# Kernel optimization log

Measured on AMD Instinct MI355X. Metric: run time of the kernel, lower is better.

The kernel has to match this reference:

```python
import jax, jax.numpy as jnp
import numpy as np

N = 50000      # nodes
E = 200000     # edges (before self-loops)
D_IN = 256
HID = 128
NEG_SLOPE = 0.2
BN_EPS = 1e-5


def _lin(k, fan_in, fan_out):
    return jax.random.normal(k, (fan_in, fan_out), jnp.float32) / np.float32(np.sqrt(fan_in))


def setup_inputs() -> dict:
    key = jax.random.key(0)
    ks = jax.random.split(key, 40)
    d = {}
    d['x'] = jax.random.normal(ks[0], (N, D_IN), jnp.float32)
    d['edge_index'] = jax.random.randint(ks[1], (2, E), 0, N, dtype=jnp.int32)
    # GAT layer 1: 256 -> 128, heads=4 (concat -> 512)
    d['W1'] = _lin(ks[2], D_IN, 4 * HID)
    d['asrc1'] = jax.random.normal(ks[3], (4, HID), jnp.float32) * 0.1
    d['adst1'] = jax.random.normal(ks[4], (4, HID), jnp.float32) * 0.1
    d['b1'] = jnp.zeros((4 * HID,), jnp.float32)
    d['g1'] = jax.random.uniform(ks[5], (4 * HID,), jnp.float32, 0.5, 1.5)
    d['be1'] = jax.random.normal(ks[6], (4 * HID,), jnp.float32) * 0.1
    d['m1'] = jax.random.normal(ks[7], (4 * HID,), jnp.float32) * 0.1
    d['v1'] = jax.random.uniform(ks[8], (4 * HID,), jnp.float32, 0.5, 1.5)
    # GAT layer 2: 512 -> 128, heads=4 (concat -> 512)
    d['W2'] = _lin(ks[9], 4 * HID, 4 * HID)
    d['asrc2'] = jax.random.normal(ks[10], (4, HID), jnp.float32) * 0.1
    d['adst2'] = jax.random.normal(ks[11], (4, HID), jnp.float32) * 0.1
    d['b2'] = jnp.zeros((4 * HID,), jnp.float32)
    d['g2'] = jax.random.uniform(ks[12], (4 * HID,), jnp.float32, 0.5, 1.5)
    d['be2'] = jax.random.normal(ks[13], (4 * HID,), jnp.float32) * 0.1
    d['m2'] = jax.random.normal(ks[14], (4 * HID,), jnp.float32) * 0.1
    d['v2'] = jax.random.uniform(ks[15], (4 * HID,), jnp.float32, 0.5, 1.5)
    # GAT layer 3: 512 -> 128, heads=1
    d['W3'] = _lin(ks[16], 4 * HID, HID)
    d['asrc3'] = jax.random.normal(ks[17], (1, HID), jnp.float32) * 0.1
    d['adst3'] = jax.random.normal(ks[18], (1, HID), jnp.float32) * 0.1
    d['b3'] = jnp.zeros((HID,), jnp.float32)
    d['g3'] = jax.random.uniform(ks[19], (HID,), jnp.float32, 0.5, 1.5)
    d['be3'] = jax.random.normal(ks[20], (HID,), jnp.float32) * 0.1
    d['m3'] = jax.random.normal(ks[21], (HID,), jnp.float32) * 0.1
    d['v3'] = jax.random.uniform(ks[22], (HID,), jnp.float32, 0.5, 1.5)
    # classifier head: 128 -> 64 -> 10
    d['Wc1'] = _lin(ks[23], HID, HID // 2)
    d['bc1'] = jnp.zeros((HID // 2,), jnp.float32)
    d['Wc2'] = _lin(ks[24], HID // 2, 10)
    d['bc2'] = jnp.zeros((10,), jnp.float32)
    return d


def _gat_layer(h, src, dst, W, asrc, adst, b, heads, ch):
    # PyG GATConv (eval mode): linear -> per-head scores -> segment softmax over dst -> aggregate
    xp = (h @ W).reshape(-1, heads, ch)                 # [N, H, C]
    e_src = (xp * asrc[None]).sum(-1)                   # [N, H]
    e_dst = (xp * adst[None]).sum(-1)                   # [N, H]
    e = jax.nn.leaky_relu(e_src[src] + e_dst[dst], NEG_SLOPE)  # [E', H]
    m = jax.lax.stop_gradient(jax.ops.segment_max(e, dst, num_segments=N))
    w = jnp.exp(e - m[dst])
    s = jax.ops.segment_sum(w, dst, num_segments=N)     # [N, H]
    alpha = w / (s[dst] + 1e-16)                        # [E', H]
    out = jax.ops.segment_sum(alpha[:, :, None] * xp[src], dst, num_segments=N)  # [N, H, C]
    return out.reshape(-1, heads * ch) + b


def _bn_relu(h, g, be, mu, var):
    return jax.nn.relu((h - mu) * jax.lax.rsqrt(var + BN_EPS) * g + be)


def reference(x, edge_index,
              W1, asrc1, adst1, b1, g1, be1, m1, v1,
              W2, asrc2, adst2, b2, g2, be2, m2, v2,
              W3, asrc3, adst3, b3, g3, be3, m3, v3,
              Wc1, bc1, Wc2, bc2):
    loop = jnp.arange(N, dtype=edge_index.dtype)
    src = jnp.concatenate([edge_index[0], loop])        # GATConv adds self-loops
    dst = jnp.concatenate([edge_index[1], loop])
    h = _bn_relu(_gat_layer(x, src, dst, W1, asrc1, adst1, b1, 4, HID), g1, be1, m1, v1)
    h = _bn_relu(_gat_layer(h, src, dst, W2, asrc2, adst2, b2, 4, HID), g2, be2, m2, v2)
    h = _bn_relu(_gat_layer(h, src, dst, W3, asrc3, adst3, b3, 1, HID), g3, be3, m3, v3)
    E_GNN = h                                           # [N, 128]
    logits = jax.nn.relu(E_GNN @ Wc1 + bc1) @ Wc2 + bc2 # [N, 10]
    P_GNN = jax.nn.softmax(logits, axis=-1)
    return (E_GNN, P_GNN)
```

## Files before the change

kernel.cpp:

```cpp
#include <hip/hip_runtime.h>
#include <math.h>

#define N_NODES 50000
#define N_EDGES 200000
#define NEG_SLOPE 0.2f
#define BN_EPS 1e-5f

#define SCAN_ELEMS 1024
#define SCAN_NB ((N_NODES + SCAN_ELEMS - 1) / SCAN_ELEMS)

typedef __attribute__((ext_vector_type(4))) float f32x4;
typedef __attribute__((ext_vector_type(8))) short bf16x8;
typedef __attribute__((ext_vector_type(8))) ushort u16x8;
typedef __attribute__((ext_vector_type(2))) ushort u16x2;

__device__ __forceinline__ ushort f2bf(float x) {
    unsigned u = __float_as_uint(x);
    u += 0x7FFFu + ((u >> 16) & 1u);
    return (ushort)(u >> 16);
}
__device__ __forceinline__ float bf2f(ushort u) {
    return __uint_as_float(((unsigned)u) << 16);
}

__global__ void k_init(int* cnt, int* off) {
    int i = blockIdx.x * blockDim.x + threadIdx.x;
    if (i < N_NODES) { cnt[i] = 1; off[i] = 1; }
}

__global__ void k_count(const int* __restrict__ ei, int* cnt) {
    int e = blockIdx.x * blockDim.x + threadIdx.x;
    if (e < N_EDGES) atomicAdd(&cnt[ei[N_EDGES + e]], 1);
}

__global__ __launch_bounds__(256) void k_scan1(const int* __restrict__ cnt,
                                               int* __restrict__ incl,
                                               int* __restrict__ partials) {
    __shared__ int sh[256];
    const int t = threadIdx.x;
    const int base = blockIdx.x * SCAN_ELEMS + t * 4;
    int v0 = 0, v1 = 0, v2 = 0, v3 = 0;
    if (base + 3 < N_NODES) {
        int4 lv = *reinterpret_cast<const int4*>(&cnt[base]);
        v0 = lv.x; v1 = lv.y; v2 = lv.z; v3 = lv.w;
    } else {
        if (base + 0 < N_NODES) v0 = cnt[base + 0];
        if (base + 1 < N_NODES) v1 = cnt[base + 1];
        if (base + 2 < N_NODES) v2 = cnt[base + 2];
        if (base + 3 < N_NODES) v3 = cnt[base + 3];
    }
    const int s1 = v0 + v1, s2 = s1 + v2, s3 = s2 + v3;
    sh[t] = s3;
    __syncthreads();
#pragma unroll
    for (int off = 1; off < 256; off <<= 1) {
        int x = (t >= off) ? sh[t - off] : 0;
        __syncthreads();
        sh[t] += x;
        __syncthreads();
    }
    const int excl = sh[t] - s3;
    if (base + 0 < N_NODES) incl[base + 0] = excl + v0;
    if (base + 1 < N_NODES) incl[base + 1] = excl + s1;
    if (base + 2 < N_NODES) incl[base + 2] = excl + s2;
    if (base + 3 < N_NODES) incl[base + 3] = excl + s3;
    if (t == 255) partials[blockIdx.x] = sh[255];
}

__global__ void k_scan2(const int* __restrict__ partials, int* __restrict__ pofs) {
    if (threadIdx.x == 0) {
        int s = 0;
        for (int b = 0; b < SCAN_NB; ++b) { pofs[b] = s; s += partials[b]; }
    }
}

__global__ void k_scan3(const int* __restrict__ incl, const int* __restrict__ pofs,
                        int* __restrict__ row_ptr) {
    int i = blockIdx.x * blockDim.x + threadIdx.x;
    if (i < N_NODES) row_ptr[i + 1] = incl[i] + pofs[i >> 10];
    if (i == 0) row_ptr[0] = 0;
}

__global__ void k_self(const int* __restrict__ row_ptr, int* colb) {
    int n = blockIdx.x * blockDim.x + threadIdx.x;
    if (n < N_NODES) colb[row_ptr[n]] = n;
}

__global__ void k_scatter(const int* __restrict__ ei, const int* __restrict__ row_ptr,
                          int* off, int* colb) {
    int e = blockIdx.x * blockDim.x + threadIdx.x;
    if (e < N_EDGES) {
        int dst = ei[N_EDGES + e];
        int p = atomicAdd(&off[dst], 1);
        colb[row_ptr[dst] + p] = ei[e];
    }
}

__global__ void k_cvt(const float* __restrict__ in, ushort* __restrict__ out, int n4) {
    int i = blockIdx.x * blockDim.x + threadIdx.x;
    if (i < n4) {
        float4 v = reinterpret_cast<const float4*>(in)[i];
        ushort4 o;
        o.x = f2bf(v.x); o.y = f2bf(v.y); o.z = f2bf(v.z); o.w = f2bf(v.w);
        reinterpret_cast<ushort4*>(out)[i] = o;
    }
}

__global__ void k_wt(const float* __restrict__ W, ushort* __restrict__ Wt, int K, int N) {
    int idx = blockIdx.x * blockDim.x + threadIdx.x;
    if (idx < K * N) {
        int n = idx / K, k = idx - n * K;
        Wt[idx] = f2bf(W[(size_t)k * N + n]);
    }
}

__global__ __launch_bounds__(512) void k_gemm256(const ushort* __restrict__ A,
                                                 const ushort* __restrict__ Bt,
                                                 ushort* __restrict__ Cb,
                                                 const float* __restrict__ asrc,
                                                 const float* __restrict__ adst,
                                                 float* __restrict__ es,
                                                 float* __restrict__ ed,
                                                 int M, int K) {
    constexpr int N = 512;
    __shared__ __align__(16) ushort L[2][12288];
    __shared__ float sles[4][128];
    __shared__ float sled[4][128];
    const int tid = threadIdx.x;
    const int wid = tid >> 6, lane = tid & 63;
    const int wm = wid >> 2, wn = wid & 3;

    const int nwg = gridDim.x;
    const int q = nwg >> 3, r = nwg & 7;
    const int xcd = blockIdx.x & 7, bidx = blockIdx.x >> 3;
    const int wg = ((xcd < r) ? xcd * (q + 1) : r * (q + 1) + (xcd - r) * q) + bidx;
    const int row0 = (wg >> 1) * 128;
    const int by = wg & 1;
    const int col0 = by * 256;

    const int sub = lane >> 2;
    const int kcol = (lane & 3) * 8;

    const ushort* gPtr[3];
    int lOfs[3];
#pragma unroll
    for (int c = 0; c < 3; ++c) {
        int chunk = wid * 3 + c;
        lOfs[c] = chunk * 512;
        if (chunk < 8) {
            int ar = row0 + chunk * 16 + sub;
            if (ar > M - 1) ar = M - 1;
            gPtr[c] = A + (size_t)ar * K + kcol;
        } else {
            int bc = chunk - 8;
            gPtr[c] = Bt + (size_t)(col0 + bc * 16 + sub) * K + kcol;
        }
    }

    const int afr = (wm * 64 + (lane & 15)) * 32 + (lane >> 4) * 8;
    const int bfr = 4096 + (wn * 64 + (lane & 15)) * 32 + (lane >> 4) * 8;

    f32x4 acc[4][4] = {};

#pragma unroll
    for (int c = 0; c < 3; ++c)
        __builtin_amdgcn_global_load_lds(
            (const __attribute__((address_space(1))) unsigned*)(gPtr[c]),
            (__attribute__((address_space(3))) unsigned*)(&L[0][lOfs[c]]), 16, 0, 0);
    __syncthreads();

    int cur = 0;
    for (int k0 = 32; k0 < K; k0 += 32) {
#pragma unroll
        for (int c = 0; c < 3; ++c)
            __builtin_amdgcn_global_load_lds(
                (const __attribute__((address_space(1))) unsigned*)(gPtr[c] + k0),
                (__attribute__((address_space(3))) unsigned*)(&L[cur ^ 1][lOfs[c]]), 16, 0, 0);
        {
            bf16x8 af[4], bg[4];
#pragma unroll
            for (int m = 0; m < 4; ++m)
                af[m] = *reinterpret_cast<const bf16x8*>(&L[cur][afr + m * 16 * 32]);
#pragma unroll
            for (int n = 0; n < 4; ++n)
                bg[n] = *reinterpret_cast<const bf16x8*>(&L[cur][bfr + n * 16 * 32]);
#pragma unroll
            for (int m = 0; m < 4; ++m)
#pragma unroll
                for (int n = 0; n < 4; ++n)
                    acc[m][n] = __builtin_amdgcn_mfma_f32_16x16x32_bf16(af[m], bg[n], acc[m][n], 0, 0, 0);
        }
        __syncthreads();
        cur ^= 1;
    }
    {
        bf16x8 af[4], bg[4];
#pragma unroll
        for (int m = 0; m < 4; ++m)
            af[m] = *reinterpret_cast<const bf16x8*>(&L[cur][afr + m * 16 * 32]);
#pragma unroll
        for (int n = 0; n < 4; ++n)
            bg[n] = *reinterpret_cast<const bf16x8*>(&L[cur][bfr + n * 16 * 32]);
#pragma unroll
        for (int m = 0; m < 4; ++m)
#pragma unroll
            for (int n = 0; n < 4; ++n)
                acc[m][n] = __builtin_amdgcn_mfma_f32_16x16x32_bf16(af[m], bg[n], acc[m][n], 0, 0, 0);
    }

    const int crow = row0 + wm * 64 + (lane >> 4) * 4;
    const int ccol = col0 + wn * 64 + (lane & 15);
#pragma unroll
    for (int m = 0; m < 4; ++m) {
#pragma unroll
        for (int j = 0; j < 4; ++j) {
            int rr = crow + m * 16 + j;
            if (rr < M) {
#pragma unroll
                for (int n = 0; n < 4; ++n)
                    Cb[(size_t)rr * N + ccol + n * 16] = f2bf(acc[m][n][j]);
            }
        }
    }

    const int head = by * 2 + (wn >> 1);
    float as_c[4], ad_c[4];
#pragma unroll
    for (int n = 0; n < 4; ++n) {
        int cl = (wn & 1) * 64 + n * 16 + (lane & 15);
        as_c[n] = asrc[head * 128 + cl];
        ad_c[n] = adst[head * 128 + cl];
    }
#pragma unroll
    for (int m = 0; m < 4; ++m) {
#pragma unroll
        for (int j = 0; j < 4; ++j) {
            float ps = acc[m][0][j] * as_c[0] + acc[m][1][j] * as_c[1] +
                       acc[m][2][j] * as_c[2] + acc[m][3][j] * as_c[3];
            float pd = acc[m][0][j] * ad_c[0] + acc[m][1][j] * ad_c[1] +
                       acc[m][2][j] * ad_c[2] + acc[m][3][j] * ad_c[3];
#pragma unroll
            for (int o = 1; o < 16; o <<= 1) {
                ps += __shfl_xor(ps, o);
                pd += __shfl_xor(pd, o);
            }
            if ((lane & 15) == 0) {
                int rl = wm * 64 + (lane >> 4) * 4 + m * 16 + j;
                sles[wn][rl] = ps;
                sled[wn][rl] = pd;
            }
        }
    }
    __syncthreads();
    if (tid < 256) {
        const int hl = tid >> 7;
        const int rl = tid & 127;
        const int rr = row0 + rl;
        if (rr < M) {
            es[(size_t)rr * 4 + by * 2 + hl] = sles[2 * hl][rl] + sles[2 * hl + 1][rl];
            ed[(size_t)rr * 4 + by * 2 + hl] = sled[2 * hl][rl] + sled[2 * hl + 1][rl];
        }
    }
}

__global__ __launch_bounds__(256) void k_gemm_bf16(const ushort* __restrict__ A,
                                                   const ushort* __restrict__ Bt,
                                                   ushort* __restrict__ Cb,
                                                   const float* __restrict__ asrc,
                                                   const float* __restrict__ adst,
                                                   float* __restrict__ es,
                                                   float* __restrict__ ed,
                                                   int M, int K, int N) {
    __shared__ __align__(16) ushort L[2][8192];
    __shared__ float sles[2][128];
    __shared__ float sled[2][128];
    const int tid = threadIdx.x;
    const int wid = tid >> 6, lane = tid & 63;
    const int wm = wid >> 1, wn = wid & 1;
    const int row0 = blockIdx.x * 128, col0 = blockIdx.y * 128;
    const int H = N >> 7;

    const int sub = lane >> 2;
    const int kcol = (lane & 3) * 8;

    const ushort* gPtr[4];
    int lOfs[4];
#pragma unroll
    for (int c = 0; c < 4; ++c) {
        int chunk = wid * 4 + c;
        lOfs[c] = chunk * 512;
        if (chunk < 8) {
            int ar = row0 + chunk * 16 + sub;
            if (ar > M - 1) ar = M - 1;
            gPtr[c] = A + (size_t)ar * K + kcol;
        } else {
            int bc = chunk - 8;
            gPtr[c] = Bt + (size_t)(col0 + bc * 16 + sub) * K + kcol;
        }
    }

    const int afr = (wm * 64 + (lane & 15)) * 32 + (lane >> 4) * 8;
    const int bfr = 4096 + (wn * 64 + (lane & 15)) * 32 + (lane >> 4) * 8;

    f32x4 acc[4][4] = {};

#pragma unroll
    for (int c = 0; c < 4; ++c)
        __builtin_amdgcn_global_load_lds(
            (const __attribute__((address_space(1))) unsigned*)(gPtr[c]),
            (__attribute__((address_space(3))) unsigned*)(&L[0][lOfs[c]]), 16, 0, 0);
    __syncthreads();

    int cur = 0;
    for (int k0 = 32; k0 < K; k0 += 32) {
#pragma unroll
        for (int c = 0; c < 4; ++c)
            __builtin_amdgcn_global_load_lds(
                (const __attribute__((address_space(1))) unsigned*)(gPtr[c] + k0),
                (__attribute__((address_space(3))) unsigned*)(&L[cur ^ 1][lOfs[c]]), 16, 0, 0);
        {
            bf16x8 af[4], bg[4];
#pragma unroll
            for (int m = 0; m < 4; ++m)
                af[m] = *reinterpret_cast<const bf16x8*>(&L[cur][afr + m * 16 * 32]);
#pragma unroll
            for (int n = 0; n < 4; ++n)
                bg[n] = *reinterpret_cast<const bf16x8*>(&L[cur][bfr + n * 16 * 32]);
#pragma unroll
            for (int m = 0; m < 4; ++m)
#pragma unroll
                for (int n = 0; n < 4; ++n)
                    acc[m][n] = __builtin_amdgcn_mfma_f32_16x16x32_bf16(af[m], bg[n], acc[m][n], 0, 0, 0);
        }
        __syncthreads();
        cur ^= 1;
    }
    {
        bf16x8 af[4], bg[4];
#pragma unroll
        for (int m = 0; m < 4; ++m)
            af[m] = *reinterpret_cast<const bf16x8*>(&L[cur][afr + m * 16 * 32]);
#pragma unroll
        for (int n = 0; n < 4; ++n)
            bg[n] = *reinterpret_cast<const bf16x8*>(&L[cur][bfr + n * 16 * 32]);
#pragma unroll
        for (int m = 0; m < 4; ++m)
#pragma unroll
            for (int n = 0; n < 4; ++n)
                acc[m][n] = __builtin_amdgcn_mfma_f32_16x16x32_bf16(af[m], bg[n], acc[m][n], 0, 0, 0);
    }

    const int crow = row0 + wm * 64 + (lane >> 4) * 4;
    const int ccol = col0 + wn * 64 + (lane & 15);
#pragma unroll
    for (int m = 0; m < 4; ++m) {
#pragma unroll
        for (int j = 0; j < 4; ++j) {
            int r = crow + m * 16 + j;
            if (r < M) {
#pragma unroll
                for (int n = 0; n < 4; ++n)
                    Cb[(size_t)r * N + ccol + n * 16] = f2bf(acc[m][n][j]);
            }
        }
    }

    float as_c[4], ad_c[4];
#pragma unroll
    for (int n = 0; n < 4; ++n) {
        int cl = wn * 64 + n * 16 + (lane & 15);
        as_c[n] = asrc[blockIdx.y * 128 + cl];
        ad_c[n] = adst[blockIdx.y * 128 + cl];
    }
#pragma unroll
    for (int m = 0; m < 4; ++m) {
#pragma unroll
        for (int j = 0; j < 4; ++j) {
            float ps = acc[m][0][j] * as_c[0] + acc[m][1][j] * as_c[1] +
                       acc[m][2][j] * as_c[2] + acc[m][3][j] * as_c[3];
            float pd = acc[m][0][j] * ad_c[0] + acc[m][1][j] * ad_c[1] +
                       acc[m][2][j] * ad_c[2] + acc[m][3][j] * ad_c[3];
#pragma unroll
            for (int o = 1; o < 16; o <<= 1) {
                ps += __shfl_xor(ps, o);
                pd += __shfl_xor(pd, o);
            }
            if ((lane & 15) == 0) {
                int rl = wm * 64 + (lane >> 4) * 4 + m * 16 + j;
                sles[wn][rl] = ps;
                sled[wn][rl] = pd;
            }
        }
    }
    __syncthreads();
    if (tid < 128) {
        int r = row0 + tid;
        if (r < M) {
            es[(size_t)r * H + blockIdx.y] = sles[0][tid] + sles[1][tid];
            ed[(size_t)r * H + blockIdx.y] = sled[0][tid] + sled[1][tid];
        }
    }
}

template <int H, bool BF16OUT>
__global__ __launch_bounds__(64) void k_agg(
    const ushort* __restrict__ xpb, const float* __restrict__ es, const float* __restrict__ ed,
    const int* __restrict__ row_ptr, const int* __restrict__ colb,
    const float* __restrict__ bias, const float* __restrict__ gg, const float* __restrict__ be,
    const float* __restrict__ mu, const float* __restrict__ var, void* __restrict__ outv) {
    constexpr int HC = H * 128;
    constexpr int CPT = HC / 64;
    constexpr int CHUNK = 128;
    constexpr int GS = (H == 4) ? 16 : 64;
    __shared__ int s_src[CHUNK];
    __shared__ float s_w[CHUNK][H];
    const int n = blockIdx.x;
    const int lane = threadIdx.x;
    const int g = (H == 4) ? (lane >> 4) : 0;
    const int gl = (H == 4) ? (lane & 15) : lane;
    const int beg = row_ptr[n], end = row_ptr[n + 1];
    const int cnt = end - beg;

    float edn[H];
#pragma unroll
    for (int h = 0; h < H; ++h) edn[h] = ed[n * H + h];

    float acc[CPT];
#pragma unroll
    for (int j = 0; j < CPT; ++j) acc[j] = 0.f;
    float m_run = -INFINITY, s_run = 0.f;
    const int ch0 = lane * CPT;
    const ushort* xb = xpb + ch0;

    for (int cbeg = 0; cbeg < cnt; cbeg += CHUNK) {
        const int cc = min(cnt - cbeg, CHUNK);
        for (int i = lane; i < cc; i += 64) {
            int src = colb[beg + cbeg + i];
            s_src[i] = src;
            if (H == 4) {
                float4 e4 = *reinterpret_cast<const float4*>(&es[src * 4]);
                float4 o;
                o.x = e4.x + edn[0]; o.x = (o.x > 0.f) ? o.x : NEG_SLOPE * o.x;
                o.y = e4.y + edn[1]; o.y = (o.y > 0.f) ? o.y : NEG_SLOPE * o.y;
                o.z = e4.z + edn[2]; o.z = (o.z > 0.f) ? o.z : NEG_SLOPE * o.z;
                o.w = e4.w + edn[3]; o.w = (o.w > 0.f) ? o.w : NEG_SLOPE * o.w;
                *reinterpret_cast<float4*>(&s_w[i][0]) = o;
            } else {
                float e = es[src] + edn[0];
                s_w[i][0] = (e > 0.f) ? e : NEG_SLOPE * e;
            }
        }
        __syncthreads();
        float cm = -INFINITY;
        for (int i = gl; i < cc; i += GS) cm = fmaxf(cm, s_w[i][g]);
#pragma unroll
        for (int o = GS >> 1; o; o >>= 1) cm = fmaxf(cm, __shfl_xor(cm, o));
        const float m_new = fmaxf(m_run, cm);
        const float scale = __expf(m_run - m_new);
        float sl = 0.f;
        for (int i = gl; i < cc; i += GS) {
            float w = __expf(s_w[i][g] - m_new);
            s_w[i][g] = w;
            sl += w;
        }
#pragma unroll
        for (int o = GS >> 1; o; o >>= 1) sl += __shfl_xor(sl, o);
        s_run = s_run * scale + sl;
        m_run = m_new;
#pragma unroll
        for (int j = 0; j < CPT; ++j) acc[j] *= scale;
        __syncthreads();
        for (int e = 0; e < cc; e += 4) {
            float w0 = s_w[e][g];
            int   p0 = s_src[e];
            float w1 = 0.f; int p1 = n;
            float w2 = 0.f; int p2 = n;
            float w3 = 0.f; int p3 = n;
            if (e + 1 < cc) { w1 = s_w[e + 1][g]; p1 = s_src[e + 1]; }
            if (e + 2 < cc) { w2 = s_w[e + 2][g]; p2 = s_src[e + 2]; }
            if (e + 3 < cc) { w3 = s_w[e + 3][g]; p3 = s_src[e + 3]; }
            if (CPT == 8) {
                u16x8 v0 = *reinterpret_cast<const u16x8*>(xb + (size_t)p0 * HC);
                u16x8 v1 = *reinterpret_cast<const u16x8*>(xb + (size_t)p1 * HC);
                u16x8 v2 = *reinterpret_cast<const u16x8*>(xb + (size_t)p2 * HC);
                u16x8 v3 = *reinterpret_cast<const u16x8*>(xb + (size_t)p3 * HC);
#pragma unroll
                for (int j = 0; j < CPT; ++j) {
                    float a = acc[j];
                    a = fmaf(w0, bf2f(v0[j]), a);
                    a = fmaf(w1, bf2f(v1[j]), a);
                    a = fmaf(w2, bf2f(v2[j]), a);
                    a = fmaf(w3, bf2f(v3[j]), a);
                    acc[j] = a;
                }
            } else {
                u16x2 v0 = *reinterpret_cast<const u16x2*>(xb + (size_t)p0 * HC);
                u16x2 v1 = *reinterpret_cast<const u16x2*>(xb + (size_t)p1 * HC);
                u16x2 v2 = *reinterpret_cast<const u16x2*>(xb + (size_t)p2 * HC);
                u16x2 v3 = *reinterpret_cast<const u16x2*>(xb + (size_t)p3 * HC);
#pragma unroll
                for (int j = 0; j < CPT; ++j) {
                    float a = acc[j];
                    a = fmaf(w0, bf2f(v0[j]), a);
                    a = fmaf(w1, bf2f(v1[j]), a);
                    a = fmaf(w2, bf2f(v2[j]), a);
                    a = fmaf(w3, bf2f(v3[j]), a);
                    acc[j] = a;
                }
            }
        }
        __syncthreads();
    }

    const float inv = 1.f / (s_run + 1e-16f);
    float vals[CPT];
#pragma unroll
    for (int j = 0; j < CPT; ++j) {
        int ch = ch0 + j;
        float val = acc[j] * inv + bias[ch];
        val = (val - mu[ch]) * (gg[ch] * rsqrtf(var[ch] + BN_EPS)) + be[ch];
        vals[j] = fmaxf(val, 0.f);
    }
    if (BF16OUT) {
        if (CPT == 8) {
            u16x8 o;
#pragma unroll
            for (int j = 0; j < CPT; ++j) o[j] = f2bf(vals[j]);
            *reinterpret_cast<u16x8*>((ushort*)outv + (size_t)n * HC + ch0) = o;
        } else {
            u16x2 o;
#pragma unroll
            for (int j = 0; j < CPT; ++j) o[j] = f2bf(vals[j]);
            *reinterpret_cast<u16x2*>((ushort*)outv + (size_t)n * HC + ch0) = o;
        }
    } else {
        float2 o = make_float2(vals[0], vals[1 % CPT]);
        *reinterpret_cast<float2*>((float*)outv + (size_t)n * HC + ch0) = o;
    }
}

#define CLS_NB 16
__global__ __launch_bounds__(256) void k_cls(const float* __restrict__ Eg,
                                             const float* __restrict__ Wc1,
                                             const float* __restrict__ bc1,
                                             const float* __restrict__ Wc2,
                                             const float* __restrict__ bc2,
                                             float* __restrict__ P) {
    __shared__ float Ws[128 * 64];
    __shared__ float W2s[64 * 10 + 16];
    __shared__ float b1s[64];
    __shared__ float e_sh[CLS_NB][128];
    __shared__ float h_sh[CLS_NB][64];
    __shared__ float l_sh[CLS_NB][10];
    const int t = threadIdx.x;
    const int n0 = blockIdx.x * CLS_NB;

    for (int i = t; i < 2048; i += 256)
        reinterpret_cast<float4*>(Ws)[i] = reinterpret_cast<const float4*>(Wc1)[i];
    for (int i = t; i < 640; i += 256) W2s[i] = Wc2[i];
    if (t < 64) b1s[t] = bc1[t];
    if (t >= 64 && t < 74) W2s[640 + t - 64] = bc2[t - 64];
    for (int i = t; i < CLS_NB * 32; i += 256) {
        int node = i >> 5, qq = i & 31;
        reinterpret_cast<float4*>(&e_sh[node][0])[qq] =
            reinterpret_cast<const float4*>(&Eg[(size_t)(n0 + node) * 128])[qq];
    }
    __syncthreads();

    {
        const int c = t & 63, ng = t >> 6;
        float acc0 = b1s[c], acc1 = b1s[c], acc2 = b1s[c], acc3 = b1s[c];
        for (int k = 0; k < 128; ++k) {
            float w = Ws[k * 64 + c];
            acc0 = fmaf(e_sh[ng * 4 + 0][k], w, acc0);
            acc1 = fmaf(e_sh[ng * 4 + 1][k], w, acc1);
            acc2 = fmaf(e_sh[ng * 4 + 2][k], w, acc2);
            acc3 = fmaf(e_sh[ng * 4 + 3][k], w, acc3);
        }
        h_sh[ng * 4 + 0][c] = fmaxf(acc0, 0.f);
        h_sh[ng * 4 + 1][c] = fmaxf(acc1, 0.f);
        h_sh[ng * 4 + 2][c] = fmaxf(acc2, 0.f);
        h_sh[ng * 4 + 3][c] = fmaxf(acc3, 0.f);
    }
    __syncthreads();
    if (t < CLS_NB * 10) {
        int node = t / 10, c = t - node * 10;
        float acc = W2s[640 + c];
        for (int k = 0; k < 64; ++k) acc = fmaf(h_sh[node][k], W2s[k * 10 + c], acc);
        l_sh[node][c] = acc;
    }
    __syncthreads();
    if (t < CLS_NB) {
        float mx = l_sh[t][0];
        for (int j = 1; j < 10; ++j) mx = fmaxf(mx, l_sh[t][j]);
        float s = 0.f;
        float ex[10];
        for (int j = 0; j < 10; ++j) { ex[j] = __expf(l_sh[t][j] - mx); s += ex[j]; }
        float inv = 1.f / s;
        for (int j = 0; j < 10; ++j) l_sh[t][j] = ex[j] * inv;
    }
    __syncthreads();
    if (t < CLS_NB * 10) {
        int node = t / 10, c = t - node * 10;
        P[(size_t)(n0 + node) * 10 + c] = l_sh[node][c];
    }
}

extern "C" void kernel_launch(void* const* d_in, const int* in_sizes, int n_in,
                              void* d_out, int out_size, void* d_ws, size_t ws_size,
                              hipStream_t stream) {
    const float* x     = (const float*)d_in[0];
    const int*   ei    = (const int*)d_in[1];
    const float* W1    = (const float*)d_in[2];
    const float* asrc1 = (const float*)d_in[3];
    const float* adst1 = (const float*)d_in[4];
    const float* b1    = (const float*)d_in[5];
    const float* gg1   = (const float*)d_in[6];
    const float* be1   = (const float*)d_in[7];
    const float* mu1   = (const float*)d_in[8];
    const float* v1    = (const float*)d_in[9];
    const float* W2    = (const float*)d_in[10];
    const float* asrc2 = (const float*)d_in[11];
    const float* adst2 = (const float*)d_in[12];
    const float* b2    = (const float*)d_in[13];
    const float* gg2   = (const float*)d_in[14];
    const float* be2   = (const float*)d_in[15];
    const float* mu2   = (const float*)d_in[16];
    const float* v2    = (const float*)d_in[17];
    const float* W3    = (const float*)d_in[18];
    const float* asrc3 = (const float*)d_in[19];
    const float* adst3 = (const float*)d_in[20];
    const float* b3    = (const float*)d_in[21];
    const float* gg3   = (const float*)d_in[22];
    const float* be3   = (const float*)d_in[23];
    const float* mu3   = (const float*)d_in[24];
    const float* v3    = (const float*)d_in[25];
    const float* Wc1   = (const float*)d_in[26];
    const float* bc1   = (const float*)d_in[27];
    const float* Wc2   = (const float*)d_in[28];
    const float* bc2   = (const float*)d_in[29];

    ushort* xpb  = (ushort*)d_ws;
    ushort* hh   = xpb + (size_t)N_NODES * 512;
    ushort* wt1  = hh + (size_t)N_NODES * 512;
    ushort* wt2  = wt1 + 512 * 256;
    ushort* wt3  = wt2 + 512 * 512;
    float*  es   = (float*)(wt3 + 128 * 512);
    float*  ed   = es + (size_t)N_NODES * 4;
    int* cnt     = (int*)(ed + (size_t)N_NODES * 4);
    int* off     = cnt + N_NODES;
    int* row_ptr = off + N_NODES;
    int* colb    = row_ptr + N_NODES + 4;
    int* incl    = colb + N_EDGES + N_NODES;
    int* partials = incl + N_NODES;
    int* pofs    = partials + SCAN_NB;

    float* Egnn = (float*)d_out;
    float* P    = Egnn + (size_t)N_NODES * 128;

    k_init<<<(N_NODES + 255) / 256, 256, 0, stream>>>(cnt, off);
    k_count<<<(N_EDGES + 255) / 256, 256, 0, stream>>>(ei, cnt);
    k_scan1<<<SCAN_NB, 256, 0, stream>>>(cnt, incl, partials);
    k_scan2<<<1, 64, 0, stream>>>(partials, pofs);
    k_scan3<<<(N_NODES + 255) / 256, 256, 0, stream>>>(incl, pofs, row_ptr);
    k_self<<<(N_NODES + 255) / 256, 256, 0, stream>>>(row_ptr, colb);
    k_scatter<<<(N_EDGES + 255) / 256, 256, 0, stream>>>(ei, row_ptr, off, colb);

    k_wt<<<(512 * 256 + 255) / 256, 256, 0, stream>>>(W1, wt1, 256, 512);
    k_wt<<<(512 * 512 + 255) / 256, 256, 0, stream>>>(W2, wt2, 512, 512);
    k_wt<<<(128 * 512 + 255) / 256, 256, 0, stream>>>(W3, wt3, 512, 128);
    {
        int n4 = N_NODES * 256 / 4;
        k_cvt<<<(n4 + 255) / 256, 256, 0, stream>>>(x, hh, n4);
    }

    const int mt = (N_NODES + 127) / 128;
    const int nwg256 = mt * 2;

    k_gemm256<<<nwg256, 512, 0, stream>>>(hh, wt1, xpb, asrc1, adst1, es, ed,
                                          N_NODES, 256);
    k_agg<4, true><<<N_NODES, 64, 0, stream>>>(xpb, es, ed, row_ptr, colb,
                                               b1, gg1, be1, mu1, v1, hh);
    k_gemm256<<<nwg256, 512, 0, stream>>>(hh, wt2, xpb, asrc2, adst2, es, ed,
                                          N_NODES, 512);
    k_agg<4, true><<<N_NODES, 64, 0, stream>>>(xpb, es, ed, row_ptr, colb,
                                               b2, gg2, be2, mu2, v2, hh);
    {
        dim3 grid(mt, 1);
        k_gemm_bf16<<<grid, 256, 0, stream>>>(hh, wt3, xpb, asrc3, adst3, es, ed,
                                              N_NODES, 512, 128);
    }
    k_agg<1, false><<<N_NODES, 64, 0, stream>>>(xpb, es, ed, row_ptr, colb,
                                                b3, gg3, be3, mu3, v3, Egnn);
    k_cls<<<(N_NODES + CLS_NB - 1) / CLS_NB, 256, 0, stream>>>(Egnn, Wc1, bc1, Wc2, bc2, P);
}
```

Before: 446.0 us.

## Fuse preprocessing kernels and remap LDS tile layout in GEMMs

Replaces the init kernel with a memset and folds the self-loop +1 into the scan. It merges scan2, scan3 and self into one kernel, with each block recomputing the partial offsets. The three weight-transpose kernels and the x conversion become a single prep kernel. It also changes the GEMM global-to-LDS load mapping and fragment offsets so lanes load 16 consecutive rows per k-chunk, which is meant to cut LDS bank conflicts, at the cost of less coalesced global reads.

Result: slower. 460.3 us (+3.2%).

```diff
diff --git a/kernel.cpp b/kernel.cpp
--- a/kernel.cpp
+++ b/kernel.cpp
@@ -21,11 +21,6 @@
 }
 __device__ __forceinline__ float bf2f(ushort u) {
     return __uint_as_float(((unsigned)u) << 16);
-}
-
-__global__ void k_init(int* cnt, int* off) {
-    int i = blockIdx.x * blockDim.x + threadIdx.x;
-    if (i < N_NODES) { cnt[i] = 1; off[i] = 1; }
 }
 
 __global__ void k_count(const int* __restrict__ ei, int* cnt) {
@@ -42,12 +37,12 @@
     int v0 = 0, v1 = 0, v2 = 0, v3 = 0;
     if (base + 3 < N_NODES) {
         int4 lv = *reinterpret_cast<const int4*>(&cnt[base]);
-        v0 = lv.x; v1 = lv.y; v2 = lv.z; v3 = lv.w;
+        v0 = lv.x + 1; v1 = lv.y + 1; v2 = lv.z + 1; v3 = lv.w + 1;
     } else {
-        if (base + 0 < N_NODES) v0 = cnt[base + 0];
-        if (base + 1 < N_NODES) v1 = cnt[base + 1];
-        if (base + 2 < N_NODES) v2 = cnt[base + 2];
-        if (base + 3 < N_NODES) v3 = cnt[base + 3];
+        if (base + 0 < N_NODES) v0 = cnt[base + 0] + 1;
+        if (base + 1 < N_NODES) v1 = cnt[base + 1] + 1;
+        if (base + 2 < N_NODES) v2 = cnt[base + 2] + 1;
+        if (base + 3 < N_NODES) v3 = cnt[base + 3] + 1;
     }
     const int s1 = v0 + v1, s2 = s1 + v2, s3 = s2 + v3;
     sh[t] = s3;
@@ -67,23 +62,21 @@
     if (t == 255) partials[blockIdx.x] = sh[255];
 }
 
-__global__ void k_scan2(const int* __restrict__ partials, int* __restrict__ pofs) {
+__global__ void k_scan3self(const int* __restrict__ incl, const int* __restrict__ partials,
+                            int* __restrict__ row_ptr, int* __restrict__ colb) {
+    __shared__ int pofs_sh[SCAN_NB];
     if (threadIdx.x == 0) {
         int s = 0;
-        for (int b = 0; b < SCAN_NB; ++b) { pofs[b] = s; s += partials[b]; }
-    }
-}
-
-__global__ void k_scan3(const int* __restrict__ incl, const int* __restrict__ pofs,
-                        int* __restrict__ row_ptr) {
+        for (int b = 0; b < SCAN_NB; ++b) { pofs_sh[b] = s; s += partials[b]; }
+    }
+    __syncthreads();
     int i = blockIdx.x * blockDim.x + threadIdx.x;
-    if (i < N_NODES) row_ptr[i + 1] = incl[i] + pofs[i >> 10];
-    if (i == 0) row_ptr[0] = 0;
-}
-
-__global__ void k_self(const int* __restrict__ row_ptr, int* colb) {
-    int n = blockIdx.x * blockDim.x + threadIdx.x;
-    if (n < N_NODES) colb[row_ptr[n]] = n;
+    if (i < N_NODES) {
+        row_ptr[i + 1] = incl[i] + pofs_sh[i >> 10];
+        int rp0 = (i == 0) ? 0 : (incl[i - 1] + pofs_sh[(i - 1) >> 10]);
+        if (i == 0) row_ptr[0] = 0;
+        colb[rp0] = i;
+    }
 }
 
 __global__ void k_scatter(const int* __restrict__ ei, const int* __restrict__ row_ptr,
@@ -92,25 +85,36 @@
     if (e < N_EDGES) {
         int dst = ei[N_EDGES + e];
         int p = atomicAdd(&off[dst], 1);
-        colb[row_ptr[dst] + p] = ei[e];
-    }
-}
-
-__global__ void k_cvt(const float* __restrict__ in, ushort* __restrict__ out, int n4) {
-    int i = blockIdx.x * blockDim.x + threadIdx.x;
-    if (i < n4) {
-        float4 v = reinterpret_cast<const float4*>(in)[i];
+        colb[row_ptr[dst] + 1 + p] = ei[e];
+    }
+}
+
+#define PREP_S1 (512 * 256)
+#define PREP_S2 (512 * 512)
+#define PREP_S3 (128 * 512)
+#define PREP_S4 (N_NODES * 256 / 4)
+__global__ void k_prep(const float* __restrict__ W1, const float* __restrict__ W2,
+                       const float* __restrict__ W3, const float* __restrict__ x,
+                       ushort* __restrict__ wt1, ushort* __restrict__ wt2,
+                       ushort* __restrict__ wt3, ushort* __restrict__ hh) {
+    int idx = blockIdx.x * blockDim.x + threadIdx.x;
+    if (idx < PREP_S1) {
+        int n = idx >> 8, k = idx & 255;
+        wt1[idx] = f2bf(W1[(size_t)k * 512 + n]);
+    } else if (idx < PREP_S1 + PREP_S2) {
+        int j = idx - PREP_S1;
+        int n = j >> 9, k = j & 511;
+        wt2[j] = f2bf(W2[(size_t)k * 512 + n]);
+    } else if (idx < PREP_S1 + PREP_S2 + PREP_S3) {
+        int j = idx - PREP_S1 - PREP_S2;
+        int n = j >> 9, k = j & 511;
+        wt3[j] = f2bf(W3[(size_t)k * 128 + n]);
+    } else if (idx < PREP_S1 + PREP_S2 + PREP_S3 + PREP_S4) {
+        int j = idx - PREP_S1 - PREP_S2 - PREP_S3;
+        float4 v = reinterpret_cast<const float4*>(x)[j];
         ushort4 o;
         o.x = f2bf(v.x); o.y = f2bf(v.y); o.z = f2bf(v.z); o.w = f2bf(v.w);
-        reinterpret_cast<ushort4*>(out)[i] = o;
-    }
-}
-
-__global__ void k_wt(const float* __restrict__ W, ushort* __restrict__ Wt, int K, int N) {
-    int idx = blockIdx.x * blockDim.x + threadIdx.x;
-    if (idx < K * N) {
-        int n = idx / K, k = idx - n * K;
-        Wt[idx] = f2bf(W[(size_t)k * N + n]);
+        reinterpret_cast<ushort4*>(hh)[j] = o;
     }
 }
 
@@ -138,8 +142,8 @@
     const int by = wg & 1;
     const int col0 = by * 256;
 
-    const int sub = lane >> 2;
-    const int kcol = (lane & 3) * 8;
+    const int sub = lane & 15;
+    const int kcol = (lane >> 4) * 8;
 
     const ushort* gPtr[3];
     int lOfs[3];
@@ -157,8 +161,8 @@
         }
     }
 
-    const int afr = (wm * 64 + (lane & 15)) * 32 + (lane >> 4) * 8;
-    const int bfr = 4096 + (wn * 64 + (lane & 15)) * 32 + (lane >> 4) * 8;
+    const int afr = wm * 2048 + (lane >> 4) * 128 + (lane & 15) * 8;
+    const int bfr = 4096 + wn * 2048 + (lane >> 4) * 128 + (lane & 15) * 8;
 
     f32x4 acc[4][4] = {};
 
@@ -180,10 +184,10 @@
             bf16x8 af[4], bg[4];
 #pragma unroll
             for (int m = 0; m < 4; ++m)
-                af[m] = *reinterpret_cast<const bf16x8*>(&L[cur][afr + m * 16 * 32]);
+                af[m] = *reinterpret_cast<const bf16x8*>(&L[cur][afr + m * 512]);
 #pragma unroll
             for (int n = 0; n < 4; ++n)
-                bg[n] = *reinterpret_cast<const bf16x8*>(&L[cur][bfr + n * 16 * 32]);
+                bg[n] = *reinterpret_cast<const bf16x8*>(&L[cur][bfr + n * 512]);
 #pragma unroll
             for (int m = 0; m < 4; ++m)
 #pragma unroll
@@ -197,10 +201,10 @@
         bf16x8 af[4], bg[4];
 #pragma unroll
         for (int m = 0; m < 4; ++m)
-            af[m] = *reinterpret_cast<const bf16x8*>(&L[cur][afr + m * 16 * 32]);
+            af[m] = *reinterpret_cast<const bf16x8*>(&L[cur][afr + m * 512]);
 #pragma unroll
         for (int n = 0; n < 4; ++n)
-            bg[n] = *reinterpret_cast<const bf16x8*>(&L[cur][bfr + n * 16 * 32]);
+            bg[n] = *reinterpret_cast<const bf16x8*>(&L[cur][bfr + n * 512]);
 #pragma unroll
         for (int m = 0; m < 4; ++m)
 #pragma unroll
@@ -280,8 +284,8 @@
     const int row0 = blockIdx.x * 128, col0 = blockIdx.y * 128;
     const int H = N >> 7;
 
-    const int sub = lane >> 2;
-    const int kcol = (lane & 3) * 8;
+    const int sub = lane & 15;
+    const int kcol = (lane >> 4) * 8;
 
     const ushort* gPtr[4];
     int lOfs[4];
@@ -299,8 +303,8 @@
         }
     }
 
-    const int afr = (wm * 64 + (lane & 15)) * 32 + (lane >> 4) * 8;
-    const int bfr = 4096 + (wn * 64 + (lane & 15)) * 32 + (lane >> 4) * 8;
+    const int afr = wm * 2048 + (lane >> 4) * 128 + (lane & 15) * 8;
+    const int bfr = 4096 + wn * 2048 + (lane >> 4) * 128 + (lane & 15) * 8;
 
     f32x4 acc[4][4] = {};
 
@@ -322,10 +326,10 @@
             bf16x8 af[4], bg[4];
 #pragma unroll
             for (int m = 0; m < 4; ++m)
-                af[m] = *reinterpret_cast<const bf16x8*>(&L[cur][afr + m * 16 * 32]);
+                af[m] = *reinterpret_cast<const bf16x8*>(&L[cur][afr + m * 512]);
 #pragma unroll
             for (int n = 0; n < 4; ++n)
-                bg[n] = *reinterpret_cast<const bf16x8*>(&L[cur][bfr + n * 16 * 32]);
+                bg[n] = *reinterpret_cast<const bf16x8*>(&L[cur][bfr + n * 512]);
 #pragma unroll
             for (int m = 0; m < 4; ++m)
 #pragma unroll
@@ -339,10 +343,10 @@
         bf16x8 af[4], bg[4];
 #pragma unroll
         for (int m = 0; m < 4; ++m)
-            af[m] = *reinterpret_cast<const bf16x8*>(&L[cur][afr + m * 16 * 32]);
+            af[m] = *reinterpret_cast<const bf16x8*>(&L[cur][afr + m * 512]);
 #pragma unroll
         for (int n = 0; n < 4; ++n)
-            bg[n] = *reinterpret_cast<const bf16x8*>(&L[cur][bfr + n * 16 * 32]);
+            bg[n] = *reinterpret_cast<const bf16x8*>(&L[cur][bfr + n * 512]);
 #pragma unroll
         for (int m = 0; m < 4; ++m)
 #pragma unroll
@@ -653,25 +657,19 @@
     int* colb    = row_ptr + N_NODES + 4;
     int* incl    = colb + N_EDGES + N_NODES;
     int* partials = incl + N_NODES;
-    int* pofs    = partials + SCAN_NB;
 
     float* Egnn = (float*)d_out;
     float* P    = Egnn + (size_t)N_NODES * 128;
 
-    k_init<<<(N_NODES + 255) / 256, 256, 0, stream>>>(cnt, off);
+    hipMemsetAsync(cnt, 0, 2 * (size_t)N_NODES * sizeof(int), stream);
     k_count<<<(N_EDGES + 255) / 256, 256, 0, stream>>>(ei, cnt);
     k_scan1<<<SCAN_NB, 256, 0, stream>>>(cnt, incl, partials);
-    k_scan2<<<1, 64, 0, stream>>>(partials, pofs);
-    k_scan3<<<(N_NODES + 255) / 256, 256, 0, stream>>>(incl, pofs, row_ptr);
-    k_self<<<(N_NODES + 255) / 256, 256, 0, stream>>>(row_ptr, colb);
+    k_scan3self<<<(N_NODES + 255) / 256, 256, 0, stream>>>(incl, partials, row_ptr, colb);
     k_scatter<<<(N_EDGES + 255) / 256, 256, 0, stream>>>(ei, row_ptr, off, colb);
 
-    k_wt<<<(512 * 256 + 255) / 256, 256, 0, stream>>>(W1, wt1, 256, 512);
-    k_wt<<<(512 * 512 + 255) / 256, 256, 0, stream>>>(W2, wt2, 512, 512);
-    k_wt<<<(128 * 512 + 255) / 256, 256, 0, stream>>>(W3, wt3, 512, 128);
     {
-        int n4 = N_NODES * 256 / 4;
-        k_cvt<<<(n4 + 255) / 256, 256, 0, stream>>>(x, hh, n4);
+        int total = PREP_S1 + PREP_S2 + PREP_S3 + PREP_S4;
+        k_prep<<<(total + 255) / 256, 256, 0, stream>>>(W1, W2, W3, x, wt1, wt2, wt3, hh);
     }
 
     const int mt = (N_NODES + 127) / 128;
```
